# Kernel optimization log

Hardware: AMD Instinct MI355X
Metric: run time of the kernel (lower is better)

Reference implementation:

```python
import jax, jax.numpy as jnp
import numpy as np

B, T, E, H = 256, 128, 300, 2048


def setup_inputs() -> dict:
    key = jax.random.key(0)
    k0, k1, k2, k3, k4 = jax.random.split(key, 5)
    s = 1.0 / np.sqrt(H)  # PyTorch LSTM init range
    return {
        "x": jax.random.normal(k0, (B, T, E), dtype=jnp.float32),
        "W_ih": jax.random.uniform(k1, (4 * H, E), dtype=jnp.float32, minval=-s, maxval=s),
        "W_hh": jax.random.uniform(k2, (4 * H, H), dtype=jnp.float32, minval=-s, maxval=s),
        "b_ih": jax.random.uniform(k3, (4 * H,), dtype=jnp.float32, minval=-s, maxval=s),
        "b_hh": jax.random.uniform(k4, (4 * H,), dtype=jnp.float32, minval=-s, maxval=s),
    }


def reference(x, W_ih, W_hh, b_ih, b_hh):
    # x: [B, T, E]; returns final hidden state h_T: [B, H]
    Bn = x.shape[0]
    Hn = W_hh.shape[1]
    # Precompute input-to-gate projection for all timesteps: [B, T, 4H]
    x_gates = jnp.einsum('bte,ge->btg', x, W_ih) + b_ih + b_hh

    def step(carry, xg_t):
        h, c = carry
        gates = xg_t + h @ W_hh.T  # [B, 4H]
        i, f, g, o = jnp.split(gates, 4, axis=-1)  # PyTorch gate order i,f,g,o
        i = jax.nn.sigmoid(i)
        f = jax.nn.sigmoid(f)
        g = jnp.tanh(g)
        o = jax.nn.sigmoid(o)
        c = f * c + i * g
        h = o * jnp.tanh(c)
        return (h, c), None

    h0 = jnp.zeros((Bn, Hn), dtype=x.dtype)
    c0 = jnp.zeros((Bn, Hn), dtype=x.dtype)
    (h_T, _), _ = jax.lax.scan(step, (h0, c0), jnp.swapaxes(x_gates, 0, 1))
    return h_T
```

## Files before the change

### kernel.cpp

```cpp
#include <hip/hip_runtime.h>

typedef unsigned short u16;
typedef unsigned int u32;
typedef __bf16 bf16x8 __attribute__((ext_vector_type(8)));
typedef float f32x4 __attribute__((ext_vector_type(4)));

#define B_ 256
#define T_ 128
#define E_ 300
#define EP 320
#define H_ 2048
#define G_ 8192

#define OFF_XBF   0UL
#define OFF_WIH   20971520UL
#define OFF_WHH   26214400UL
#define OFF_BIAS  59768832UL
#define OFF_HBUF  59801600UL
#define OFF_BAR   61898752UL

#define GLDS16(gp, sp)                                                    \
  __builtin_amdgcn_global_load_lds(                                       \
      (__attribute__((address_space(1))) void*)(void*)(gp),               \
      (__attribute__((address_space(3))) void*)(sp), 16, 0, 0)
#define GLDS16C(gp, sp)                                                   \
  __builtin_amdgcn_global_load_lds(                                       \
      (__attribute__((address_space(1))) void*)(void*)(gp),               \
      (__attribute__((address_space(3))) void*)(sp), 16, 0, 17)

__device__ __forceinline__ u16 f2bf(float f) {
  u32 u = __builtin_bit_cast(u32, f);
  return (u16)((u + 0x7FFFu + ((u >> 16) & 1u)) >> 16);
}
__device__ __forceinline__ float sigm_f(float x) {
  return __builtin_amdgcn_rcpf(1.0f + __expf(-x));
}
__device__ __forceinline__ float tanh_f(float x) {
  return 1.0f - 2.0f * __builtin_amdgcn_rcpf(1.0f + __expf(2.0f * x));
}

__global__ void prep_kernel(const float* __restrict__ x, const float* __restrict__ Wih,
                            const float* __restrict__ Whh, const float* __restrict__ bih,
                            const float* __restrict__ bhh, u16* __restrict__ xbf,
                            u16* __restrict__ wihb, u16* __restrict__ whhb,
                            float* __restrict__ biasc, u32* __restrict__ bar) {
  const long NX = (long)T_ * B_ * EP;
  const long NWIH = (long)G_ * EP;
  const long NWHH = (long)G_ * H_;
  const long NBS = G_;
  const long NBAR = T_;
  const long total = NX + NWIH + NWHH + NBS + NBAR;
  for (long q = (long)blockIdx.x * blockDim.x + threadIdx.x; q < total;
       q += (long)gridDim.x * blockDim.x) {
    long r = q;
    if (r < NX) {
      int t = (int)(r / (B_ * EP));
      int rem = (int)(r % (B_ * EP));
      int b = rem / EP, e = rem % EP;
      float v = (e < E_) ? x[((long)b * T_ + t) * E_ + e] : 0.0f;
      xbf[r] = f2bf(v);
    } else if ((r -= NX) < NWIH) {
      int n = (int)(r / EP), e = (int)(r % EP);
      wihb[r] = f2bf((e < E_) ? Wih[(long)n * E_ + e] : 0.0f);
    } else if ((r -= NWIH) < NWHH) {
      whhb[r] = f2bf(Whh[r]);
    } else if ((r -= NWHH) < NBS) {
      biasc[r] = bih[r] + bhh[r];
    } else {
      r -= NBS;
      bar[r] = 0;
    }
  }
}

__global__ void __launch_bounds__(256, 1)
lstm_kernel(const u16* __restrict__ xbf, const u16* __restrict__ wihb,
            const u16* __restrict__ whhb, const float* __restrict__ biasc,
            u16* __restrict__ hbuf, u32* __restrict__ bar, float* __restrict__ out) {
  __shared__ __align__(16) u16 As[2][64 * 64];
  __shared__ __align__(16) u16 Bs[2][128 * 64];

  const int tid = threadIdx.x;
  const int l = tid & 63;
  const int w = tid >> 6;
  const int wr = w >> 1, wj = w & 1;
  const int bid = blockIdx.x;
  const int b0 = (bid >> 6) << 6;
  const int j0 = (bid & 63) << 5;
  const int jc = j0 + (wj << 4) + (l & 15);
  const int cgl = (tid & 7) ^ ((tid >> 3) & 7);

  const float bi = biasc[jc];
  const float bff = biasc[2048 + jc];
  const float bg = biasc[4096 + jc];
  const float bo = biasc[6144 + jc];

  float cst[2][4];
#pragma unroll
  for (int mi = 0; mi < 2; ++mi)
#pragma unroll
    for (int r = 0; r < 4; ++r) cst[mi][r] = 0.0f;

  auto stageA = [&](const u16* srcA, int strA, int kk, int p, bool coh) {
    u16* Ad = &As[p][w * 512];
#pragma unroll
    for (int i = 0; i < 2; ++i) {
      int slot = i * 256 + tid;
      const u16* g = srcA + (size_t)(slot >> 3) * strA + kk + cgl * 8;
      if (coh) { GLDS16C(g, Ad + i * 2048); } else { GLDS16(g, Ad + i * 2048); }
    }
  };
  auto stageB = [&](const u16* srcB, int strB, int kk, int p) {
    u16* Bd = &Bs[p][w * 512];
#pragma unroll
    for (int i = 0; i < 4; ++i) {
      int slot = i * 256 + tid;
      int nl = slot >> 3;
      int grow = ((nl >> 5) << 11) + j0 + (nl & 31);
      const u16* g = srcB + (size_t)grow * strB + kk + cgl * 8;
      GLDS16(g, Bd + i * 2048);
    }
  };

#pragma unroll 1
  for (int t = 0; t < T_; ++t) {
    const u16* hcur = hbuf + (size_t)(t & 1) * (B_ * H_) + (size_t)b0 * H_;
    u16* hnxt = hbuf + (size_t)((t + 1) & 1) * (B_ * H_);
    const u16* xsrc = xbf + (size_t)t * (B_ * EP) + (size_t)b0 * EP;

    f32x4 acc[2][4];
#pragma unroll
    for (int mi = 0; mi < 2; ++mi)
#pragma unroll
      for (int g = 0; g < 4; ++g) acc[mi][g] = (f32x4){0.f, 0.f, 0.f, 0.f};

    auto compute = [&](int p) {
#pragma unroll
      for (int k2 = 0; k2 < 2; ++k2) {
        int cp = ((k2 << 2) + (l >> 4)) ^ (l & 7);
        const u16* ap = &As[p][((wr << 5) + (l & 15)) * 64 + cp * 8];
        bf16x8 a0 = *(const bf16x8*)ap;
        bf16x8 a1 = *(const bf16x8*)(ap + 1024);
        const u16* bp = &Bs[p][((wj << 4) + (l & 15)) * 64 + cp * 8];
        bf16x8 bv0 = *(const bf16x8*)bp;
        bf16x8 bv1 = *(const bf16x8*)(bp + 2048);
        bf16x8 bv2 = *(const bf16x8*)(bp + 4096);
        bf16x8 bv3 = *(const bf16x8*)(bp + 6144);
        acc[0][0] = __builtin_amdgcn_mfma_f32_16x16x32_bf16(a0, bv0, acc[0][0], 0, 0, 0);
        acc[0][1] = __builtin_amdgcn_mfma_f32_16x16x32_bf16(a0, bv1, acc[0][1], 0, 0, 0);
        acc[0][2] = __builtin_amdgcn_mfma_f32_16x16x32_bf16(a0, bv2, acc[0][2], 0, 0, 0);
        acc[0][3] = __builtin_amdgcn_mfma_f32_16x16x32_bf16(a0, bv3, acc[0][3], 0, 0, 0);
        acc[1][0] = __builtin_amdgcn_mfma_f32_16x16x32_bf16(a1, bv0, acc[1][0], 0, 0, 0);
        acc[1][1] = __builtin_amdgcn_mfma_f32_16x16x32_bf16(a1, bv1, acc[1][1], 0, 0, 0);
        acc[1][2] = __builtin_amdgcn_mfma_f32_16x16x32_bf16(a1, bv2, acc[1][2], 0, 0, 0);
        acc[1][3] = __builtin_amdgcn_mfma_f32_16x16x32_bf16(a1, bv3, acc[1][3], 0, 0, 0);
      }
    };

    int p = 0;
    stageA(xsrc, EP, 0, 0, false);
    stageB(wihb, EP, 0, 0);
    __syncthreads();
#pragma unroll 1
    for (int kx = 0; kx < 5; ++kx) {
      if (kx < 4) {
        stageA(xsrc, EP, (kx + 1) << 6, p ^ 1, false);
        stageB(wihb, EP, (kx + 1) << 6, p ^ 1);
      }
      compute(p);
      __syncthreads();
      p ^= 1;
    }

    if (t > 0) {
      if (tid == 0) {
        while (__hip_atomic_load(&bar[t - 1], __ATOMIC_RELAXED,
                                 __HIP_MEMORY_SCOPE_AGENT) < 256u)
          __builtin_amdgcn_s_sleep(2);
      }
      __syncthreads();
      stageA(hcur, H_, 0, p, true);
      stageB(whhb, H_, 0, p);
      __syncthreads();
#pragma unroll 1
      for (int kh = 0; kh < 32; ++kh) {
        if (kh < 31) {
          stageA(hcur, H_, (kh + 1) << 6, p ^ 1, true);
          stageB(whhb, H_, (kh + 1) << 6, p ^ 1);
        }
        compute(p);
        __syncthreads();
        p ^= 1;
      }
    }

#pragma unroll
    for (int mi = 0; mi < 2; ++mi) {
#pragma unroll
      for (int r = 0; r < 4; ++r) {
        float ig = sigm_f(acc[mi][0][r] + bi);
        float fg = sigm_f(acc[mi][1][r] + bff);
        float gg = tanh_f(acc[mi][2][r] + bg);
        float og = sigm_f(acc[mi][3][r] + bo);
        float c = fg * cst[mi][r] + ig * gg;
        cst[mi][r] = c;
        float h = og * tanh_f(c);
        int row = b0 + (wr << 5) + (mi << 4) + ((l >> 4) << 2) + r;
        if (t < T_ - 1) {
          u16 hv = f2bf(h);
          u16* hp = hnxt + (size_t)row * H_ + jc;
          asm volatile("global_store_short %0, %1, off sc0 sc1"
                       :: "v"(hp), "v"((u32)hv) : "memory");
        } else {
          out[(size_t)row * H_ + jc] = h;
        }
      }
    }

    if (t < T_ - 1) {
      __builtin_amdgcn_s_waitcnt(0);
      __syncthreads();
      if (tid == 0)
        __hip_atomic_fetch_add(&bar[t], 1u, __ATOMIC_RELAXED,
                               __HIP_MEMORY_SCOPE_AGENT);
    }
  }
}

extern "C" void kernel_launch(void* const* d_in, const int* in_sizes, int n_in,
                              void* d_out, int out_size, void* d_ws, size_t ws_size,
                              hipStream_t stream) {
  const float* x = (const float*)d_in[0];
  const float* Wih = (const float*)d_in[1];
  const float* Whh = (const float*)d_in[2];
  const float* bih = (const float*)d_in[3];
  const float* bhh = (const float*)d_in[4];
  char* ws = (char*)d_ws;
  u16* xbf = (u16*)(ws + OFF_XBF);
  u16* wihb = (u16*)(ws + OFF_WIH);
  u16* whhb = (u16*)(ws + OFF_WHH);
  float* biasc = (float*)(ws + OFF_BIAS);
  u16* hbuf = (u16*)(ws + OFF_HBUF);
  u32* bar = (u32*)(ws + OFF_BAR);
  float* out = (float*)d_out;

  hipLaunchKernelGGL(prep_kernel, dim3(2048), dim3(256), 0, stream,
                     x, Wih, Whh, bih, bhh, xbf, wihb, whhb, biasc, bar);

  void* args[] = {(void*)&xbf, (void*)&wihb, (void*)&whhb,
                  (void*)&biasc, (void*)&hbuf, (void*)&bar, (void*)&out};
  hipLaunchCooperativeKernel((void*)lstm_kernel, dim3(256), dim3(256), args, 0, stream);
}
```

Measured before the change: 3.789 ms.

## Keep per-block weight slices resident in LDS across all timesteps of persistent LSTM

Re-partitions the persistent LSTM so each of the 256 blocks owns 8 hidden units across all 256 batch rows, and loads its slice of W_hh and W_ih (pre-packed into MFMA fragment order by the prep kernel) into LDS once, about 150 KB. The goal is to stop re-streaming the full recurrent weight matrix from global memory on every timestep. Activations h and x are now read straight from global/L2 into registers instead of being staged through double-buffered LDS. Gates are recombined across lanes with shuffles, and half the lanes store h. The cost is very high LDS use, every block reading the whole h state each step, and reliance on a plain acquire fence in place of the coherent-load flag for h visibility.

```diff
diff --git a/kernel.cpp b/kernel.cpp
--- a/kernel.cpp
+++ b/kernel.cpp
@@ -13,8 +13,8 @@
 #define G_ 8192
 
 #define OFF_XBF   0UL
-#define OFF_WIH   20971520UL
-#define OFF_WHH   26214400UL
+#define OFF_WPK   20971520UL
+#define OFF_WIP   54525952UL
 #define OFF_BIAS  59768832UL
 #define OFF_HBUF  59801600UL
 #define OFF_BAR   61898752UL
@@ -23,10 +23,6 @@
   __builtin_amdgcn_global_load_lds(                                       \
       (__attribute__((address_space(1))) void*)(void*)(gp),               \
       (__attribute__((address_space(3))) void*)(sp), 16, 0, 0)
-#define GLDS16C(gp, sp)                                                   \
-  __builtin_amdgcn_global_load_lds(                                       \
-      (__attribute__((address_space(1))) void*)(void*)(gp),               \
-      (__attribute__((address_space(3))) void*)(sp), 16, 0, 17)
 
 __device__ __forceinline__ u16 f2bf(float f) {
   u32 u = __builtin_bit_cast(u32, f);
@@ -42,14 +38,14 @@
 __global__ void prep_kernel(const float* __restrict__ x, const float* __restrict__ Wih,
                             const float* __restrict__ Whh, const float* __restrict__ bih,
                             const float* __restrict__ bhh, u16* __restrict__ xbf,
-                            u16* __restrict__ wihb, u16* __restrict__ whhb,
+                            u16* __restrict__ wpk, u16* __restrict__ wip,
                             float* __restrict__ biasc, u32* __restrict__ bar) {
   const long NX = (long)T_ * B_ * EP;
-  const long NWIH = (long)G_ * EP;
-  const long NWHH = (long)G_ * H_;
+  const long NWPK = 256L * 65536L;
+  const long NWIP = 256L * 10240L;
   const long NBS = G_;
   const long NBAR = T_;
-  const long total = NX + NWIH + NWHH + NBS + NBAR;
+  const long total = NX + NWPK + NWIP + NBS + NBAR;
   for (long q = (long)blockIdx.x * blockDim.x + threadIdx.x; q < total;
        q += (long)gridDim.x * blockDim.x) {
     long r = q;
@@ -59,12 +55,23 @@
       int b = rem / EP, e = rem % EP;
       float v = (e < E_) ? x[((long)b * T_ + t) * E_ + e] : 0.0f;
       xbf[r] = f2bf(v);
-    } else if ((r -= NX) < NWIH) {
-      int n = (int)(r / EP), e = (int)(r % EP);
-      wihb[r] = f2bf((e < E_) ? Wih[(long)n * E_ + e] : 0.0f);
-    } else if ((r -= NWIH) < NWHH) {
-      whhb[r] = f2bf(Whh[r]);
-    } else if ((r -= NWHH) < NBS) {
+    } else if ((r -= NX) < NWPK) {
+      int blk = (int)(r >> 16);
+      int qq = (int)(r & 65535);
+      int e = qq & 7, ln = (qq >> 3) & 63, f = (qq >> 9) & 1, k2 = qq >> 10;
+      int gate = f * 2 + ((ln >> 3) & 1);
+      int grow = gate * H_ + blk * 8 + (ln & 7);
+      int k = k2 * 32 + ((ln >> 4) & 3) * 8 + e;
+      wpk[r] = f2bf(Whh[(long)grow * H_ + k]);
+    } else if ((r -= NWPK) < NWIP) {
+      int blk = (int)(r / 10240);
+      int qq = (int)(r % 10240);
+      int e = qq & 7, ln = (qq >> 3) & 63, f = (qq >> 9) & 1, k2 = qq >> 10;
+      int gate = f * 2 + ((ln >> 3) & 1);
+      int grow = gate * H_ + blk * 8 + (ln & 7);
+      int k = k2 * 32 + ((ln >> 4) & 3) * 8 + e;
+      wip[r] = f2bf((k < E_) ? Wih[(long)grow * E_ + k] : 0.0f);
+    } else if ((r -= NWIP) < NBS) {
       biasc[r] = bih[r] + bhh[r];
     } else {
       r -= NBS;
@@ -74,102 +81,79 @@
 }
 
 __global__ void __launch_bounds__(256, 1)
-lstm_kernel(const u16* __restrict__ xbf, const u16* __restrict__ wihb,
-            const u16* __restrict__ whhb, const float* __restrict__ biasc,
+lstm_kernel(const u16* __restrict__ xbf, const u16* __restrict__ wpk,
+            const u16* __restrict__ wip, const float* __restrict__ biasc,
             u16* __restrict__ hbuf, u32* __restrict__ bar, float* __restrict__ out) {
-  __shared__ __align__(16) u16 As[2][64 * 64];
-  __shared__ __align__(16) u16 Bs[2][128 * 64];
+  __shared__ __align__(16) u16 Wl[65536];
+  __shared__ __align__(16) u16 WIl[10240];
 
   const int tid = threadIdx.x;
   const int l = tid & 63;
   const int w = tid >> 6;
-  const int wr = w >> 1, wj = w & 1;
   const int bid = blockIdx.x;
-  const int b0 = (bid >> 6) << 6;
-  const int j0 = (bid & 63) << 5;
-  const int jc = j0 + (wj << 4) + (l & 15);
-  const int cgl = (tid & 7) ^ ((tid >> 3) & 7);
+  const int rowbase = w << 6;
+  const int rl = l & 15;
+  const int kb = (l >> 4) << 3;
+  const int c = l & 7;
+  const int jc = (bid << 3) + c;
+  const int half = (l >> 3) & 1;
+
+  {
+    const u16* wsrc = wpk + ((size_t)bid << 16);
+    const u16* wisrc = wip + (size_t)bid * 10240;
+    u16* wdst = Wl + (w << 9);
+    u16* widst = WIl + (w << 9);
+#pragma unroll
+    for (int i = 0; i < 32; ++i)
+      GLDS16(wsrc + (i << 11) + (tid << 3), wdst + (i << 11));
+#pragma unroll
+    for (int i = 0; i < 5; ++i)
+      GLDS16(wisrc + (i << 11) + (tid << 3), widst + (i << 11));
+    __syncthreads();
+  }
 
   const float bi = biasc[jc];
-  const float bff = biasc[2048 + jc];
-  const float bg = biasc[4096 + jc];
-  const float bo = biasc[6144 + jc];
-
-  float cst[2][4];
-#pragma unroll
-  for (int mi = 0; mi < 2; ++mi)
-#pragma unroll
-    for (int r = 0; r < 4; ++r) cst[mi][r] = 0.0f;
-
-  auto stageA = [&](const u16* srcA, int strA, int kk, int p, bool coh) {
-    u16* Ad = &As[p][w * 512];
-#pragma unroll
-    for (int i = 0; i < 2; ++i) {
-      int slot = i * 256 + tid;
-      const u16* g = srcA + (size_t)(slot >> 3) * strA + kk + cgl * 8;
-      if (coh) { GLDS16C(g, Ad + i * 2048); } else { GLDS16(g, Ad + i * 2048); }
-    }
-  };
-  auto stageB = [&](const u16* srcB, int strB, int kk, int p) {
-    u16* Bd = &Bs[p][w * 512];
-#pragma unroll
-    for (int i = 0; i < 4; ++i) {
-      int slot = i * 256 + tid;
-      int nl = slot >> 3;
-      int grow = ((nl >> 5) << 11) + j0 + (nl & 31);
-      const u16* g = srcB + (size_t)grow * strB + kk + cgl * 8;
-      GLDS16(g, Bd + i * 2048);
-    }
-  };
+  const float bff = biasc[H_ + jc];
+  const float bg = biasc[2 * H_ + jc];
+  const float bo = biasc[3 * H_ + jc];
+
+  float cst[4][4];
+#pragma unroll
+  for (int rf = 0; rf < 4; ++rf)
+#pragma unroll
+    for (int r = 0; r < 4; ++r) cst[rf][r] = 0.0f;
 
 #pragma unroll 1
   for (int t = 0; t < T_; ++t) {
-    const u16* hcur = hbuf + (size_t)(t & 1) * (B_ * H_) + (size_t)b0 * H_;
+    const u16* hcur = hbuf + (size_t)(t & 1) * (B_ * H_);
     u16* hnxt = hbuf + (size_t)((t + 1) & 1) * (B_ * H_);
-    const u16* xsrc = xbf + (size_t)t * (B_ * EP) + (size_t)b0 * EP;
-
-    f32x4 acc[2][4];
-#pragma unroll
-    for (int mi = 0; mi < 2; ++mi)
-#pragma unroll
-      for (int g = 0; g < 4; ++g) acc[mi][g] = (f32x4){0.f, 0.f, 0.f, 0.f};
-
-    auto compute = [&](int p) {
-#pragma unroll
-      for (int k2 = 0; k2 < 2; ++k2) {
-        int cp = ((k2 << 2) + (l >> 4)) ^ (l & 7);
-        const u16* ap = &As[p][((wr << 5) + (l & 15)) * 64 + cp * 8];
-        bf16x8 a0 = *(const bf16x8*)ap;
-        bf16x8 a1 = *(const bf16x8*)(ap + 1024);
-        const u16* bp = &Bs[p][((wj << 4) + (l & 15)) * 64 + cp * 8];
-        bf16x8 bv0 = *(const bf16x8*)bp;
-        bf16x8 bv1 = *(const bf16x8*)(bp + 2048);
-        bf16x8 bv2 = *(const bf16x8*)(bp + 4096);
-        bf16x8 bv3 = *(const bf16x8*)(bp + 6144);
-        acc[0][0] = __builtin_amdgcn_mfma_f32_16x16x32_bf16(a0, bv0, acc[0][0], 0, 0, 0);
-        acc[0][1] = __builtin_amdgcn_mfma_f32_16x16x32_bf16(a0, bv1, acc[0][1], 0, 0, 0);
-        acc[0][2] = __builtin_amdgcn_mfma_f32_16x16x32_bf16(a0, bv2, acc[0][2], 0, 0, 0);
-        acc[0][3] = __builtin_amdgcn_mfma_f32_16x16x32_bf16(a0, bv3, acc[0][3], 0, 0, 0);
-        acc[1][0] = __builtin_amdgcn_mfma_f32_16x16x32_bf16(a1, bv0, acc[1][0], 0, 0, 0);
-        acc[1][1] = __builtin_amdgcn_mfma_f32_16x16x32_bf16(a1, bv1, acc[1][1], 0, 0, 0);
-        acc[1][2] = __builtin_amdgcn_mfma_f32_16x16x32_bf16(a1, bv2, acc[1][2], 0, 0, 0);
-        acc[1][3] = __builtin_amdgcn_mfma_f32_16x16x32_bf16(a1, bv3, acc[1][3], 0, 0, 0);
-      }
-    };
-
-    int p = 0;
-    stageA(xsrc, EP, 0, 0, false);
-    stageB(wihb, EP, 0, 0);
-    __syncthreads();
-#pragma unroll 1
-    for (int kx = 0; kx < 5; ++kx) {
-      if (kx < 4) {
-        stageA(xsrc, EP, (kx + 1) << 6, p ^ 1, false);
-        stageB(wihb, EP, (kx + 1) << 6, p ^ 1);
-      }
-      compute(p);
-      __syncthreads();
-      p ^= 1;
+
+    f32x4 acc[4][2];
+#pragma unroll
+    for (int rf = 0; rf < 4; ++rf) {
+      acc[rf][0] = (f32x4){0.f, 0.f, 0.f, 0.f};
+      acc[rf][1] = (f32x4){0.f, 0.f, 0.f, 0.f};
+    }
+
+    {
+      const u16* xa = xbf + (size_t)t * (B_ * EP) + (size_t)(rowbase + rl) * EP + kb;
+#pragma unroll 2
+      for (int k2 = 0; k2 < 10; ++k2) {
+        bf16x8 b0 = *(const bf16x8*)(WIl + (k2 << 10) + (l << 3));
+        bf16x8 b1 = *(const bf16x8*)(WIl + (k2 << 10) + 512 + (l << 3));
+        bf16x8 a0 = *(const bf16x8*)(xa + (k2 << 5));
+        bf16x8 a1 = *(const bf16x8*)(xa + 16 * EP + (k2 << 5));
+        bf16x8 a2 = *(const bf16x8*)(xa + 32 * EP + (k2 << 5));
+        bf16x8 a3 = *(const bf16x8*)(xa + 48 * EP + (k2 << 5));
+        acc[0][0] = __builtin_amdgcn_mfma_f32_16x16x32_bf16(a0, b0, acc[0][0], 0, 0, 0);
+        acc[0][1] = __builtin_amdgcn_mfma_f32_16x16x32_bf16(a0, b1, acc[0][1], 0, 0, 0);
+        acc[1][0] = __builtin_amdgcn_mfma_f32_16x16x32_bf16(a1, b0, acc[1][0], 0, 0, 0);
+        acc[1][1] = __builtin_amdgcn_mfma_f32_16x16x32_bf16(a1, b1, acc[1][1], 0, 0, 0);
+        acc[2][0] = __builtin_amdgcn_mfma_f32_16x16x32_bf16(a2, b0, acc[2][0], 0, 0, 0);
+        acc[2][1] = __builtin_amdgcn_mfma_f32_16x16x32_bf16(a2, b1, acc[2][1], 0, 0, 0);
+        acc[3][0] = __builtin_amdgcn_mfma_f32_16x16x32_bf16(a3, b0, acc[3][0], 0, 0, 0);
+        acc[3][1] = __builtin_amdgcn_mfma_f32_16x16x32_bf16(a3, b1, acc[3][1], 0, 0, 0);
+      }
     }
 
     if (t > 0) {
@@ -179,40 +163,57 @@
           __builtin_amdgcn_s_sleep(2);
       }
       __syncthreads();
-      stageA(hcur, H_, 0, p, true);
-      stageB(whhb, H_, 0, p);
-      __syncthreads();
-#pragma unroll 1
-      for (int kh = 0; kh < 32; ++kh) {
-        if (kh < 31) {
-          stageA(hcur, H_, (kh + 1) << 6, p ^ 1, true);
-          stageB(whhb, H_, (kh + 1) << 6, p ^ 1);
-        }
-        compute(p);
-        __syncthreads();
-        p ^= 1;
-      }
-    }
-
-#pragma unroll
-    for (int mi = 0; mi < 2; ++mi) {
+      __builtin_amdgcn_fence(__ATOMIC_ACQUIRE, "agent");
+
+      const u16* ha = hcur + (size_t)(rowbase + rl) * H_ + kb;
+#pragma unroll 4
+      for (int k2 = 0; k2 < 64; ++k2) {
+        bf16x8 b0 = *(const bf16x8*)(Wl + (k2 << 10) + (l << 3));
+        bf16x8 b1 = *(const bf16x8*)(Wl + (k2 << 10) + 512 + (l << 3));
+        bf16x8 a0 = *(const bf16x8*)(ha + (k2 << 5));
+        bf16x8 a1 = *(const bf16x8*)(ha + 16 * H_ + (k2 << 5));
+        bf16x8 a2 = *(const bf16x8*)(ha + 32 * H_ + (k2 << 5));
+        bf16x8 a3 = *(const bf16x8*)(ha + 48 * H_ + (k2 << 5));
+        acc[0][0] = __builtin_amdgcn_mfma_f32_16x16x32_bf16(a0, b0, acc[0][0], 0, 0, 0);
+        acc[0][1] = __builtin_amdgcn_mfma_f32_16x16x32_bf16(a0, b1, acc[0][1], 0, 0, 0);
+        acc[1][0] = __builtin_amdgcn_mfma_f32_16x16x32_bf16(a1, b0, acc[1][0], 0, 0, 0);
+        acc[1][1] = __builtin_amdgcn_mfma_f32_16x16x32_bf16(a1, b1, acc[1][1], 0, 0, 0);
+        acc[2][0] = __builtin_amdgcn_mfma_f32_16x16x32_bf16(a2, b0, acc[2][0], 0, 0, 0);
+        acc[2][1] = __builtin_amdgcn_mfma_f32_16x16x32_bf16(a2, b1, acc[2][1], 0, 0, 0);
+        acc[3][0] = __builtin_amdgcn_mfma_f32_16x16x32_bf16(a3, b0, acc[3][0], 0, 0, 0);
+        acc[3][1] = __builtin_amdgcn_mfma_f32_16x16x32_bf16(a3, b1, acc[3][1], 0, 0, 0);
+      }
+    }
+
+#pragma unroll
+    for (int rf = 0; rf < 4; ++rf) {
 #pragma unroll
       for (int r = 0; r < 4; ++r) {
-        float ig = sigm_f(acc[mi][0][r] + bi);
-        float fg = sigm_f(acc[mi][1][r] + bff);
-        float gg = tanh_f(acc[mi][2][r] + bg);
-        float og = sigm_f(acc[mi][3][r] + bo);
-        float c = fg * cst[mi][r] + ig * gg;
-        cst[mi][r] = c;
-        float h = og * tanh_f(c);
-        int row = b0 + (wr << 5) + (mi << 4) + ((l >> 4) << 2) + r;
+        float v0 = acc[rf][0][r];
+        float v1 = acc[rf][1][r];
+        float p0 = __shfl_xor(v0, 8);
+        float p1 = __shfl_xor(v1, 8);
+        float iv = half ? p0 : v0;
+        float fv = half ? v0 : p0;
+        float gv = half ? p1 : v1;
+        float ov = half ? v1 : p1;
+        float ig = sigm_f(iv + bi);
+        float fg = sigm_f(fv + bff);
+        float gg = tanh_f(gv + bg);
+        float og = sigm_f(ov + bo);
+        float cc = fg * cst[rf][r] + ig * gg;
+        cst[rf][r] = cc;
+        float h = og * tanh_f(cc);
+        int row = rowbase + (rf << 4) + ((l >> 4) << 2) + r;
         if (t < T_ - 1) {
-          u16 hv = f2bf(h);
-          u16* hp = hnxt + (size_t)row * H_ + jc;
-          asm volatile("global_store_short %0, %1, off sc0 sc1"
-                       :: "v"(hp), "v"((u32)hv) : "memory");
+          if ((l & 8) == 0) {
+            u16 hv = f2bf(h);
+            u16* hp = hnxt + (size_t)row * H_ + jc;
+            asm volatile("global_store_short %0, %1, off sc0 sc1"
+                         :: "v"(hp), "v"((u32)hv) : "memory");
+          }
         } else {
-          out[(size_t)row * H_ + jc] = h;
+          if ((l & 8) == 0) out[(size_t)row * H_ + jc] = h;
         }
       }
     }
@@ -237,17 +238,17 @@
   const float* bhh = (const float*)d_in[4];
   char* ws = (char*)d_ws;
   u16* xbf = (u16*)(ws + OFF_XBF);
-  u16* wihb = (u16*)(ws + OFF_WIH);
-  u16* whhb = (u16*)(ws + OFF_WHH);
+  u16* wpk = (u16*)(ws + OFF_WPK);
+  u16* wip = (u16*)(ws + OFF_WIP);
   float* biasc = (float*)(ws + OFF_BIAS);
   u16* hbuf = (u16*)(ws + OFF_HBUF);
   u32* bar = (u32*)(ws + OFF_BAR);
   float* out = (float*)d_out;
 
   hipLaunchKernelGGL(prep_kernel, dim3(2048), dim3(256), 0, stream,
-                     x, Wih, Whh, bih, bhh, xbf, wihb, whhb, biasc, bar);
-
-  void* args[] = {(void*)&xbf, (void*)&wihb, (void*)&whhb,
+                     x, Wih, Whh, bih, bhh, xbf, wpk, wip, biasc, bar);
+
+  void* args[] = {(void*)&xbf, (void*)&wpk, (void*)&wip,
                   (void*)&biasc, (void*)&hbuf, (void*)&bar, (void*)&out};
   hipLaunchCooperativeKernel((void*)lstm_kernel, dim3(256), dim3(256), args, 0, stream);
 }
```

New measurement: 7.230 ms. 90.8% more time.

## Deepen LDS pipeline to four stages with explicit vmcnt waits

Applied to the files above, without the earlier changes.

Grows the shared-memory staging buffers from two to four stages. Both the input projection and the recurrent GEMM now prefetch three K-tiles ahead, and each tile is gated by an explicit s_waitcnt vmcnt count plus a raw barrier instead of __syncthreads. The W_hh tiles for the first stages are issued before the cross-block spin wait, so weight loads overlap the synchronisation. The cost is more LDS per block, and the hand-tuned vmcnt counts are fragile: they must exactly match the number of outstanding loads per stage.

```diff
diff --git a/kernel.cpp b/kernel.cpp
--- a/kernel.cpp
+++ b/kernel.cpp
@@ -77,8 +77,8 @@
 lstm_kernel(const u16* __restrict__ xbf, const u16* __restrict__ wihb,
             const u16* __restrict__ whhb, const float* __restrict__ biasc,
             u16* __restrict__ hbuf, u32* __restrict__ bar, float* __restrict__ out) {
-  __shared__ __align__(16) u16 As[2][64 * 64];
-  __shared__ __align__(16) u16 Bs[2][128 * 64];
+  __shared__ __align__(16) u16 As[4][64 * 64];
+  __shared__ __align__(16) u16 Bs[4][128 * 64];
 
   const int tid = threadIdx.x;
   const int l = tid & 63;
@@ -120,6 +120,24 @@
       const u16* g = srcB + (size_t)grow * strB + kk + cgl * 8;
       GLDS16(g, Bd + i * 2048);
     }
+  };
+
+  auto lead = [&](int vm) {
+    switch (vm) {
+      case 18: asm volatile("s_waitcnt vmcnt(18)" ::: "memory"); break;
+      case 14: asm volatile("s_waitcnt vmcnt(14)" ::: "memory"); break;
+      case 12: asm volatile("s_waitcnt vmcnt(12)" ::: "memory"); break;
+      case 10: asm volatile("s_waitcnt vmcnt(10)" ::: "memory"); break;
+      case 6:  asm volatile("s_waitcnt vmcnt(6)"  ::: "memory"); break;
+      default: asm volatile("s_waitcnt vmcnt(0)"  ::: "memory"); break;
+    }
+    __builtin_amdgcn_s_barrier();
+    __builtin_amdgcn_sched_barrier(0);
+  };
+  auto trail = [&]() {
+    asm volatile("s_waitcnt lgkmcnt(0)" ::: "memory");
+    __builtin_amdgcn_sched_barrier(0);
+    __builtin_amdgcn_s_barrier();
   };
 
 #pragma unroll 1
@@ -157,40 +175,40 @@
       }
     };
 
-    int p = 0;
-    stageA(xsrc, EP, 0, 0, false);
-    stageB(wihb, EP, 0, 0);
-    __syncthreads();
-#pragma unroll 1
-    for (int kx = 0; kx < 5; ++kx) {
-      if (kx < 4) {
-        stageA(xsrc, EP, (kx + 1) << 6, p ^ 1, false);
-        stageB(wihb, EP, (kx + 1) << 6, p ^ 1);
-      }
-      compute(p);
-      __syncthreads();
-      p ^= 1;
-    }
+    stageA(xsrc, EP, 0, 0, false);   stageB(wihb, EP, 0, 0);
+    stageA(xsrc, EP, 64, 1, false);  stageB(wihb, EP, 64, 1);
+    stageA(xsrc, EP, 128, 2, false); stageB(wihb, EP, 128, 2);
+    stageA(xsrc, EP, 192, 3, false); stageB(wihb, EP, 192, 3);
+    lead(18); compute(0); trail();
+    stageA(xsrc, EP, 256, 0, false); stageB(wihb, EP, 256, 0);
+    lead(18); compute(1); trail();
+    lead(12); compute(2); trail();
+    lead(6);  compute(3); trail();
+    lead(0);  compute(0); trail();
 
     if (t > 0) {
+      stageB(whhb, H_, 0, 0);
+      stageB(whhb, H_, 64, 1);
+      stageB(whhb, H_, 128, 2);
       if (tid == 0) {
         while (__hip_atomic_load(&bar[t - 1], __ATOMIC_RELAXED,
                                  __HIP_MEMORY_SCOPE_AGENT) < 256u)
           __builtin_amdgcn_s_sleep(2);
       }
       __syncthreads();
-      stageA(hcur, H_, 0, p, true);
-      stageB(whhb, H_, 0, p);
-      __syncthreads();
+      stageA(hcur, H_, 0, 0, true);
+      stageA(hcur, H_, 64, 1, true);
+      stageA(hcur, H_, 128, 2, true);
 #pragma unroll 1
       for (int kh = 0; kh < 32; ++kh) {
-        if (kh < 31) {
-          stageA(hcur, H_, (kh + 1) << 6, p ^ 1, true);
-          stageB(whhb, H_, (kh + 1) << 6, p ^ 1);
+        if (kh < 29) {
+          stageA(hcur, H_, (kh + 3) << 6, (kh + 3) & 3, true);
+          stageB(whhb, H_, (kh + 3) << 6, (kh + 3) & 3);
         }
-        compute(p);
-        __syncthreads();
-        p ^= 1;
+        int vm = (kh == 0) ? 10 : (kh == 1) ? 14 : (kh < 29) ? 18 : (31 - kh) * 6;
+        lead(vm);
+        compute(kh & 3);
+        trail();
       }
     }
 
```

Result: no change. 3.728 ms (-1.6%).
